# Kernel tuning notes

Hardware: AMD Instinct MI355X
Metric: run time of the kernel (lower is better)

Reference implementation:

```python
import jax, jax.numpy as jnp
import numpy as np

POOL = 7  # RoIPooling output size (7,7)


def roi_pool(x, img, rois):
    """RoIPool matching the torch loop: scale rois to feature coords, truncate to int,
    take inclusive slice [y1:y2+1, x1:x2+1] and AdaptiveMaxPool2d((7,7)).
    x: [1,C,H,W], img: [1,3,h,w], rois: [N,4] (x1,y1,x2,y2 in image coords).
    Returns [N,C,7,7]."""
    _, C, H, W = x.shape
    h_img, w_img = img.shape[2], img.shape[3]
    scale = jnp.array([W / w_img, H / h_img, W / w_img, H / h_img], jnp.float32)
    r = (rois * scale).astype(jnp.int32)  # .long() truncation (coords >= 0)
    x1 = jnp.clip(r[:, 0], 0, W - 1)
    y1 = jnp.clip(r[:, 1], 0, H - 1)
    x2 = jnp.clip(r[:, 2], 0, W - 1)
    y2 = jnp.clip(r[:, 3], 0, H - 1)
    ww = x2 - x1 + 1  # inclusive slice width
    hh = y2 - y1 + 1
    i = jnp.arange(POOL)
    # AdaptiveMaxPool bin boundaries: start=floor(i*L/7), end=ceil((i+1)*L/7)  -> [N,7]
    col_s = x1[:, None] + (i[None, :] * ww[:, None]) // POOL
    col_e = x1[:, None] + ((i[None, :] + 1) * ww[:, None] + POOL - 1) // POOL
    row_s = y1[:, None] + (i[None, :] * hh[:, None]) // POOL
    row_e = y1[:, None] + ((i[None, :] + 1) * hh[:, None] + POOL - 1) // POOL
    wpos = jnp.arange(W)
    hpos = jnp.arange(H)
    colmask = (wpos[None, None, :] >= col_s[:, :, None]) & (wpos[None, None, :] < col_e[:, :, None])  # [N,7,W]
    rowmask = (hpos[None, None, :] >= row_s[:, :, None]) & (hpos[None, None, :] < row_e[:, :, None])  # [N,7,H]
    feat = x[0]  # [C,H,W]
    neg = jnp.asarray(jnp.finfo(feat.dtype).min, feat.dtype)
    def per_roi(masks):
        rm, cm = masks  # [7,H], [7,W]
        # separable max over the rectangular bin: cols first, then rows
        t = jnp.max(jnp.where(cm[None, None, :, :], feat[:, :, None, :], neg), axis=-1)  # [C,H,7]
        return jnp.max(jnp.where(rm[None, :, :, None], t[:, None, :, :], neg), axis=2)  # [C,7,7]
    return jax.lax.map(per_roi, (rowmask, colmask))  # [N,C,7,7]


def setup_inputs() -> dict:
    key = jax.random.key(0)
    ks = jax.random.split(key, 10)
    C, H, W = 512, 50, 50
    h_img, w_img = 800, 800
    N = 512
    num_classes = 20
    x = jax.random.normal(ks[0], (1, C, H, W), jnp.float32)
    img = jnp.zeros((1, 3, h_img, w_img), jnp.float32)
    bx = jax.random.uniform(ks[1], (N,), minval=0.0, maxval=w_img - 320.0)
    by = jax.random.uniform(ks[2], (N,), minval=0.0, maxval=h_img - 320.0)
    bw = jax.random.uniform(ks[3], (N,), minval=32.0, maxval=320.0)
    bh = jax.random.uniform(ks[4], (N,), minval=32.0, maxval=320.0)
    rois = jnp.stack([bx, by, bx + bw, by + bh], axis=1).astype(jnp.float32)
    D = C * POOL * POOL  # 25088
    W1 = jax.random.normal(ks[5], (D, 4096), jnp.float32) / np.sqrt(D)
    b1 = jnp.zeros((4096,), jnp.float32)
    W2 = jax.random.normal(ks[6], (4096, 4096), jnp.float32) / np.sqrt(4096)
    b2 = jnp.zeros((4096,), jnp.float32)
    Wcls = jax.random.normal(ks[7], (4096, num_classes + 1), jnp.float32) / np.sqrt(4096)
    bcls = jnp.zeros((num_classes + 1,), jnp.float32)
    Wreg = jax.random.normal(ks[8], (4096, 4 * (num_classes + 1)), jnp.float32) / np.sqrt(4096)
    breg = jnp.zeros((4 * (num_classes + 1),), jnp.float32)
    return {"x": x, "img": img, "rois": rois, "W1": W1, "b1": b1, "W2": W2,
            "b2": b2, "Wcls": Wcls, "bcls": bcls, "Wreg": Wreg, "breg": breg}


def reference(x, img, rois, W1, b1, W2, b2, Wcls, bcls, Wreg, breg):
    pooled = roi_pool(x, img, rois)                 # [N,C,7,7]
    f = pooled.reshape(pooled.shape[0], -1)          # flatten -> [N,25088]
    f = jax.nn.relu(f @ W1 + b1)                     # fc_head layer 1
    f = jax.nn.relu(f @ W2 + b2)                     # fc_head layer 2
    y_cls = f @ Wcls + bcls                          # [N, num_classes+1]
    y_reg = f @ Wreg + breg                          # [N, 4*(num_classes+1)]
    return (y_cls, y_reg)
```

## Files before the change

kernel.cpp:

```cpp
#include <hip/hip_runtime.h>


typedef __attribute__((ext_vector_type(8))) __bf16 bf16x8;
typedef __attribute__((ext_vector_type(4))) float f32x4;
typedef __attribute__((ext_vector_type(4))) unsigned int u32x4;

#define N_ROIS 512
#define FH 50
#define FW 50
#define KK1 25088
#define D1 4096
#define BK 32

__device__ __forceinline__ void gll16(const void* g, void* l) {
  __builtin_amdgcn_global_load_lds(
      (const __attribute__((address_space(1))) void*)g,
      (__attribute__((address_space(3))) void*)l, 16, 0, 0);
}

__global__ __launch_bounds__(256) void roipool_kernel(
    const float* __restrict__ x, const float* __restrict__ rois,
    __bf16* __restrict__ pooled) {
  const int bid = blockIdx.x;
  const int roi = bid >> 3;
  const int cg = bid & 7;
  const float s = 0.0625f;
  const float r0 = rois[roi * 4 + 0], r1 = rois[roi * 4 + 1];
  const float r2 = rois[roi * 4 + 2], r3 = rois[roi * 4 + 3];
  int x1 = (int)(r0 * s); x1 = min(max(x1, 0), FW - 1);
  int y1 = (int)(r1 * s); y1 = min(max(y1, 0), FH - 1);
  int x2 = (int)(r2 * s); x2 = min(max(x2, 0), FW - 1);
  int y2 = (int)(r3 * s); y2 = min(max(y2, 0), FH - 1);
  const int ww = x2 - x1 + 1, hh = y2 - y1 + 1;
  __shared__ int cs[7], ce[7], rs[7], re[7];
  if (threadIdx.x < 7) {
    int i = threadIdx.x;
    cs[i] = x1 + (i * ww) / 7;
    ce[i] = x1 + ((i + 1) * ww + 6) / 7;
    rs[i] = y1 + (i * hh) / 7;
    re[i] = y1 + ((i + 1) * hh + 6) / 7;
  }
  __syncthreads();
  for (int idx = threadIdx.x; idx < 64 * 49; idx += 256) {
    int cl = idx / 49;
    int p = idx - cl * 49;
    int py = p / 7, px = p - py * 7;
    const int c = cg * 64 + cl;
    const float* base = x + (size_t)c * (FH * FW);
    float m = -3.402823466e38f;
    for (int y = rs[py]; y < re[py]; ++y) {
      const float* rowp = base + y * FW;
      for (int xx = cs[px]; xx < ce[px]; ++xx) m = fmaxf(m, rowp[xx]);
    }
    pooled[(size_t)roi * KK1 + c * 49 + p] = (__bf16)m;
  }
}

template <typename OutT>
__global__ __launch_bounds__(256, 3) void gemm_pipe(
    const __bf16* __restrict__ A, const float* __restrict__ B,
    OutT* __restrict__ part, int N, int K, int kslice, int npad, int zshift) {
  __shared__ unsigned int Bu[2][2048];
  __shared__ __bf16 A_lds[2][128 * 32];
  const int tid = threadIdx.x;
  const int lane = tid & 63;
  const int w = tid >> 6;
  const int wm = w >> 1, wn = w & 1;
  const int bid = blockIdx.x;
  const int z = bid & ((1 << zshift) - 1);
  const int rest = bid >> zshift;
  const int mt = rest & 3;
  const int nt = rest >> 2;
  const int n0 = nt * 128;
  const int m0 = mt * 128;
  const int kbeg = z * kslice;
  const int niters = kslice / BK;
  const int fr = lane & 15;
  const int ks = lane >> 4;

  f32x4 acc[4][4];
#pragma unroll
  for (int i = 0; i < 4; ++i)
#pragma unroll
    for (int j = 0; j < 4; ++j) acc[i][j] = (f32x4){0.f, 0.f, 0.f, 0.f};

  const int aswz = (lane & 3) ^ ((lane >> 2) & 3) ^ ((lane >> 4) & 3);
  const __bf16* Asrc =
      A + (size_t)(m0 + w * 32 + (lane >> 2)) * K + kbeg + aswz * 8;
  const int aslot = ks ^ ((fr & 3) ^ ((fr >> 2) & 3));

  const int bc = tid & 127;
  const int bh = tid >> 7;
  const float* Bgsrc = B + n0 + bc;
  const int bswz = (bc >> 2) & 3;
  const int widx0 = bc * 16 + (((2 * bh) ^ bswz) << 2);
  const int widx1 = bc * 16 + (((2 * bh + 1) ^ bswz) << 2);

  float g0, g1, g2, g3, g4, g5, g6, g7, g8, g9, ga, gb, gc, gd, ge, gf;

#define LOAD_BG(t)                                                        \
  {                                                                       \
    int off = (t) * BK;                                                   \
    if (off >= kslice) off = 0;             \
    const float* p = Bgsrc + (size_t)(kbeg + off + 16 * bh) * N;          \
    g0 = p[0];            g1 = p[(size_t)N];                              \
    g2 = p[(size_t)2*N];  g3 = p[(size_t)3*N];                            \
    g4 = p[(size_t)4*N];  g5 = p[(size_t)5*N];                            \
    g6 = p[(size_t)6*N];  g7 = p[(size_t)7*N];                            \
    g8 = p[(size_t)8*N];  g9 = p[(size_t)9*N];                            \
    ga = p[(size_t)10*N]; gb = p[(size_t)11*N];                           \
    gc = p[(size_t)12*N]; gd = p[(size_t)13*N];                           \
    ge = p[(size_t)14*N]; gf = p[(size_t)15*N];                           \
  }

#define WRITE_BU(buf)                                                     \
  {                                                                       \
    union { __bf16 h[2]; unsigned int u; } q;                             \
    unsigned int u0, u1, u2, u3, u4, u5, u6, u7;                          \
    q.h[0] = (__bf16)g0; q.h[1] = (__bf16)g1; u0 = q.u;                   \
    q.h[0] = (__bf16)g2; q.h[1] = (__bf16)g3; u1 = q.u;                   \
    q.h[0] = (__bf16)g4; q.h[1] = (__bf16)g5; u2 = q.u;                   \
    q.h[0] = (__bf16)g6; q.h[1] = (__bf16)g7; u3 = q.u;                   \
    q.h[0] = (__bf16)g8; q.h[1] = (__bf16)g9; u4 = q.u;                   \
    q.h[0] = (__bf16)ga; q.h[1] = (__bf16)gb; u5 = q.u;                   \
    q.h[0] = (__bf16)gc; q.h[1] = (__bf16)gd; u6 = q.u;                   \
    q.h[0] = (__bf16)ge; q.h[1] = (__bf16)gf; u7 = q.u;                   \
    *(u32x4*)&Bu[buf][widx0] = (u32x4){u0, u1, u2, u3};                   \
    *(u32x4*)&Bu[buf][widx1] = (u32x4){u4, u5, u6, u7};                   \
  }

#define STAGE_A(t)                                                        \
  {                                                                       \
    int off = (t) * BK;                                                   \
    if (off >= kslice) off = 0;    \
    _Pragma("unroll") for (int i = 0; i < 2; ++i) {                       \
      gll16((const void*)(Asrc + (size_t)(i * 16) * K + off),             \
            (void*)&A_lds[(t) & 1][(w * 32 + i * 16) * 32]);              \
    }                                                                     \
  }

  LOAD_BG(0);
  STAGE_A(0);
  WRITE_BU(0);
  __syncthreads();

  for (int it = 0; it < niters; ++it) {
    const int cur = it & 1;
    const bool more = (it + 1) < niters;
    if (more) {
      LOAD_BG(it + 1);
      STAGE_A(it + 1);
    }
    bf16x8 af[4];
    {
      const __bf16* al = &A_lds[cur][0];
#pragma unroll
      for (int mf = 0; mf < 4; ++mf)
        af[mf] = *(const bf16x8*)(al + (wm * 64 + mf * 16 + fr) * 32 +
                                  aslot * 8);
    }
    const unsigned int* bl = &Bu[cur][0];
#pragma unroll
    for (int nf = 0; nf < 4; ++nf) {
      const int c = wn * 64 + nf * 16 + fr;
      bf16x8 bfr = *(const bf16x8*)((const char*)bl + c * 64 +
                                    (ks ^ ((c >> 2) & 3)) * 16);
#pragma unroll
      for (int mf = 0; mf < 4; ++mf)
        acc[mf][nf] = __builtin_amdgcn_mfma_f32_16x16x32_bf16(
            af[mf], bfr, acc[mf][nf], 0, 0, 0);
    }
    if (more) WRITE_BU(cur ^ 1);
    __syncthreads();
  }
#undef STAGE_A
#undef WRITE_BU
#undef LOAD_BG

  const int r0 = ks * 4;
  OutT* pbase = part + (size_t)z * 512 * npad;
#pragma unroll
  for (int mf = 0; mf < 4; ++mf)
#pragma unroll
    for (int nf = 0; nf < 4; ++nf) {
      const int col = n0 + wn * 64 + nf * 16 + fr;
#pragma unroll
      for (int r = 0; r < 4; ++r) {
        const int row = m0 + wm * 64 + mf * 16 + r0 + r;
        pbase[(size_t)row * npad + col] = (OutT)acc[mf][nf][r];
      }
    }
}

template <typename OutT>
__global__ __launch_bounds__(256, 1) void gemm_small(
    const __bf16* __restrict__ A, const float* __restrict__ B,
    OutT* __restrict__ part, int N, int K, int kslice, int npad, int zshift) {
  const int tid = threadIdx.x;
  const int lane = tid & 63;
  const int w = tid >> 6;
  const int bid = blockIdx.x;
  const int z = bid & ((1 << zshift) - 1);
  const int n0 = (bid >> zshift) * 64;
  const int kbeg = z * kslice;
  const int niters = kslice / BK;
  const int kmax = kbeg + kslice;
  const int fr = lane & 15;
  const int ks = lane >> 4;
  const int m0 = w * 128;
  const bool fullN = (n0 + 64) <= N;

  f32x4 acc[8][4];
#pragma unroll
  for (int i = 0; i < 8; ++i)
#pragma unroll
    for (int j = 0; j < 4; ++j) acc[i][j] = (f32x4){0.f, 0.f, 0.f, 0.f};

  const __bf16* Abase = A + (size_t)(m0 + fr) * K + ks * 8;
  const size_t Astride = (size_t)16 * K;
  const float* Bbase = B + n0 + fr;

  bf16x8 afA[8], afB[8];
  float bA[32], bB[32];

#define LOAD_A(D, t)                                                     \
  {                                                                      \
    int kk = kbeg + (t) * BK;                                            \
    if (kk >= kmax) kk = kbeg;                                           \
    const __bf16* ap = Abase + kk;                                       \
    _Pragma("unroll") for (int i = 0; i < 8; ++i)                        \
        D[i] = *(const bf16x8*)(ap + (size_t)i * Astride);               \
  }

#define LOAD_B(S, t)                                                     \
  {                                                                      \
    int kg = kbeg + (t) * BK;                                            \
    if (kg >= kmax) kg = kbeg;                                           \
    const float* p = Bbase + (size_t)(kg + ks * 8) * N;                  \
    if (fullN) {                                                         \
      _Pragma("unroll") for (int e = 0; e < 8; ++e) {                    \
        _Pragma("unroll") for (int nf = 0; nf < 4; ++nf)                 \
            S[e * 4 + nf] = p[nf * 16];                                  \
        p += N;                                                          \
      }                                                                  \
    } else {                                                             \
      _Pragma("unroll") for (int e = 0; e < 8; ++e) {                    \
        _Pragma("unroll") for (int nf = 0; nf < 4; ++nf)                 \
            S[e * 4 + nf] =                                              \
                (n0 + nf * 16 + fr < N) ? p[nf * 16] : 0.f;              \
        p += N;                                                          \
      }                                                                  \
    }                                                                    \
  }

#define BODY(it, CA, NA, CB)                                             \
  {                                                                      \
    bf16x8 bfr[4];                                                       \
    _Pragma("unroll") for (int e = 0; e < 8; ++e)                        \
        _Pragma("unroll") for (int nf = 0; nf < 4; ++nf)                 \
            bfr[nf][e] = (__bf16)CB[e * 4 + nf];                         \
    LOAD_B(CB, (it) + 2);                                                \
    LOAD_A(NA, (it) + 1);                                                \
    _Pragma("unroll") for (int nf = 0; nf < 4; ++nf)                     \
        _Pragma("unroll") for (int mf = 0; mf < 8; ++mf)                 \
            acc[mf][nf] = __builtin_amdgcn_mfma_f32_16x16x32_bf16(       \
                CA[mf], bfr[nf], acc[mf][nf], 0, 0, 0);                  \
  }

  LOAD_A(afA, 0);
  LOAD_B(bA, 0);
  LOAD_B(bB, 1);
  for (int it = 0; it < niters; it += 2) {
    BODY(it, afA, afB, bA);
    BODY(it + 1, afB, afA, bB);
  }
#undef BODY
#undef LOAD_B
#undef LOAD_A

  const int r0 = ks * 4;
  OutT* pbase = part + (size_t)z * 512 * npad;
#pragma unroll
  for (int mf = 0; mf < 8; ++mf)
#pragma unroll
    for (int nf = 0; nf < 4; ++nf) {
      const int col = n0 + nf * 16 + fr;
#pragma unroll
      for (int r = 0; r < 4; ++r) {
        const int row = m0 + mf * 16 + r0 + r;
        pbase[(size_t)row * npad + col] = (OutT)acc[mf][nf][r];
      }
    }
}

__global__ __launch_bounds__(256) void reduce_relu_kernel(
    const __bf16* __restrict__ part, const float* __restrict__ bias,
    __bf16* __restrict__ out, int nsplit) {
  const int idx = blockIdx.x * 256 + threadIdx.x;
  const int flat = idx * 8;
  if (flat >= 512 * 4096) return;
  float s[8];
#pragma unroll
  for (int j = 0; j < 8; ++j) s[j] = 0.f;
  for (int sp = 0; sp < nsplit; ++sp) {
    bf16x8 v = *(const bf16x8*)(part + (size_t)sp * (512 * 4096) + flat);
#pragma unroll
    for (int j = 0; j < 8; ++j) s[j] += (float)v[j];
  }
  const int nb = flat & 4095;
  bf16x8 o;
#pragma unroll
  for (int j = 0; j < 8; ++j) {
    float v = s[j] + bias[nb + j];
    o[j] = (__bf16)(v > 0.f ? v : 0.f);
  }
  *(bf16x8*)(out + flat) = o;
}

__global__ __launch_bounds__(256) void reduce_out_kernel(
    const float* __restrict__ pc, const float* __restrict__ pr,
    const float* __restrict__ bcls, const float* __restrict__ breg,
    float* __restrict__ out, int nsplit) {
  const int gid = blockIdx.x * 256 + threadIdx.x;
  if (gid >= 512 * 105) return;
  if (gid < 512 * 21) {
    const int m = gid / 21, j = gid - m * 21;
    float s = bcls[j];
    for (int sp = 0; sp < nsplit; ++sp)
      s += pc[(size_t)sp * 512 * 128 + m * 128 + j];
    out[gid] = s;
  } else {
    const int g = gid - 512 * 21;
    const int m = g / 84, j = g - m * 84;
    float s = breg[j];
    for (int sp = 0; sp < nsplit; ++sp)
      s += pr[(size_t)sp * 512 * 128 + m * 128 + j];
    out[gid] = s;
  }
}

extern "C" void kernel_launch(void* const* d_in, const int* in_sizes, int n_in,
                              void* d_out, int out_size, void* d_ws, size_t ws_size,
                              hipStream_t stream) {
  (void)in_sizes; (void)n_in; (void)out_size;
  const float* x    = (const float*)d_in[0];
  const float* rois = (const float*)d_in[2];
  const float* W1   = (const float*)d_in[3];
  const float* b1   = (const float*)d_in[4];
  const float* W2   = (const float*)d_in[5];
  const float* b2   = (const float*)d_in[6];
  const float* Wcls = (const float*)d_in[7];
  const float* bcls = (const float*)d_in[8];
  const float* Wreg = (const float*)d_in[9];
  const float* breg = (const float*)d_in[10];
  float* out = (float*)d_out;

  const size_t pooled_b = (size_t)512 * KK1 * 2;
  const size_t act_b = (size_t)512 * D1 * 2;
  const size_t need8 = pooled_b + (size_t)8 * act_b + 2 * act_b;
  const int ns = (ws_size >= need8) ? 8 : 2;
  const int zshift = (ns == 8) ? 3 : 1;

  char* ws = (char*)d_ws;
  __bf16* pooled = (__bf16*)ws;
  __bf16* part1 = (__bf16*)(ws + pooled_b);
  __bf16* f1 = (__bf16*)(ws + pooled_b + (size_t)ns * act_b);
  __bf16* f2 = (__bf16*)(ws + pooled_b + (size_t)ns * act_b + act_b);
  __bf16* part2 = (__bf16*)ws;
  float* pcls = (float*)ws;
  float* preg = (float*)(ws + (size_t)64 * 512 * 128 * 4);

  roipool_kernel<<<N_ROIS * 8, 256, 0, stream>>>(x, rois, pooled);

  gemm_pipe<__bf16><<<32 * 4 * ns, 256, 0, stream>>>(
      pooled, W1, part1, 4096, KK1, KK1 / ns, 4096, zshift);
  reduce_relu_kernel<<<1024, 256, 0, stream>>>(part1, b1, f1, ns);

  gemm_pipe<__bf16><<<32 * 4 * ns, 256, 0, stream>>>(
      f1, W2, part2, 4096, 4096, 4096 / ns, 4096, zshift);
  reduce_relu_kernel<<<1024, 256, 0, stream>>>(part2, b2, f2, ns);

  gemm_small<float><<<64, 256, 0, stream>>>(
      f2, Wcls, pcls, 21, 4096, 64, 128, 6);
  gemm_small<float><<<128, 256, 0, stream>>>(
      f2, Wreg, preg, 84, 4096, 64, 128, 6);
  reduce_out_kernel<<<(512 * 105 + 255) / 256, 256, 0, stream>>>(
      pcls, preg, bcls, breg, out, 64);
}
```

Baseline: 371.3 us.

## Retile FC GEMMs to full-M 512x64 blocks so each weight column is read once

The big FC GEMM kernel now uses 512-thread blocks that each cover all 512 rows (ROIs) and a 64-wide column strip, instead of 128x128 tiles across four M-tiles. The point is that each fp32 weight element is loaded from global memory and converted to bf16 only once, not four times, which cuts the dominant weight traffic. The cost is a larger A tile in LDS, fewer blocks per CU (launch bounds 512,1), and a grid of 64*ns blocks, which may lower occupancy and latency hiding.

```diff
diff --git a/kernel.cpp b/kernel.cpp
--- a/kernel.cpp
+++ b/kernel.cpp
@@ -3,7 +3,6 @@
 
 typedef __attribute__((ext_vector_type(8))) __bf16 bf16x8;
 typedef __attribute__((ext_vector_type(4))) float f32x4;
-typedef __attribute__((ext_vector_type(4))) unsigned int u32x4;
 
 #define N_ROIS 512
 #define FH 50
@@ -57,22 +56,17 @@
 }
 
 template <typename OutT>
-__global__ __launch_bounds__(256, 3) void gemm_pipe(
+__global__ __launch_bounds__(512, 1) void gemm_pipe(
     const __bf16* __restrict__ A, const float* __restrict__ B,
     OutT* __restrict__ part, int N, int K, int kslice, int npad, int zshift) {
-  __shared__ unsigned int Bu[2][2048];
-  __shared__ __bf16 A_lds[2][128 * 32];
+  __shared__ __bf16 A_lds[2][512 * 32];
+  __shared__ unsigned int Bu[2][1024];
   const int tid = threadIdx.x;
   const int lane = tid & 63;
   const int w = tid >> 6;
-  const int wm = w >> 1, wn = w & 1;
   const int bid = blockIdx.x;
   const int z = bid & ((1 << zshift) - 1);
-  const int rest = bid >> zshift;
-  const int mt = rest & 3;
-  const int nt = rest >> 2;
-  const int n0 = nt * 128;
-  const int m0 = mt * 128;
+  const int n0 = (bid >> zshift) * 64;
   const int kbeg = z * kslice;
   const int niters = kslice / BK;
   const int fr = lane & 15;
@@ -86,56 +80,44 @@
 
   const int aswz = (lane & 3) ^ ((lane >> 2) & 3) ^ ((lane >> 4) & 3);
   const __bf16* Asrc =
-      A + (size_t)(m0 + w * 32 + (lane >> 2)) * K + kbeg + aswz * 8;
+      A + (size_t)(w * 64 + (lane >> 2)) * K + kbeg + aswz * 8;
   const int aslot = ks ^ ((fr & 3) ^ ((fr >> 2) & 3));
 
-  const int bc = tid & 127;
-  const int bh = tid >> 7;
+  const int bc = tid & 63;
+  const int bh = tid >> 6;
   const float* Bgsrc = B + n0 + bc;
-  const int bswz = (bc >> 2) & 3;
-  const int widx0 = bc * 16 + (((2 * bh) ^ bswz) << 2);
-  const int widx1 = bc * 16 + (((2 * bh + 1) ^ bswz) << 2);
-
-  float g0, g1, g2, g3, g4, g5, g6, g7, g8, g9, ga, gb, gc, gd, ge, gf;
+  const int kp0 = 2 * bh;
+  const int widx = bc * 16 + (((kp0 >> 2) ^ ((bc >> 2) & 3)) << 2) + (kp0 & 3);
+
+  float g0, g1, g2, g3;
 
 #define LOAD_BG(t)                                                        \
   {                                                                       \
     int off = (t) * BK;                                                   \
     if (off >= kslice) off = 0;             \
-    const float* p = Bgsrc + (size_t)(kbeg + off + 16 * bh) * N;          \
-    g0 = p[0];            g1 = p[(size_t)N];                              \
-    g2 = p[(size_t)2*N];  g3 = p[(size_t)3*N];                            \
-    g4 = p[(size_t)4*N];  g5 = p[(size_t)5*N];                            \
-    g6 = p[(size_t)6*N];  g7 = p[(size_t)7*N];                            \
-    g8 = p[(size_t)8*N];  g9 = p[(size_t)9*N];                            \
-    ga = p[(size_t)10*N]; gb = p[(size_t)11*N];                           \
-    gc = p[(size_t)12*N]; gd = p[(size_t)13*N];                           \
-    ge = p[(size_t)14*N]; gf = p[(size_t)15*N];                           \
+    const float* p = Bgsrc + (size_t)(kbeg + off + 4 * bh) * N;           \
+    g0 = p[0];                                                            \
+    g1 = p[(size_t)N];                                                    \
+    g2 = p[(size_t)2 * N];                                                \
+    g3 = p[(size_t)3 * N];                                                \
   }
 
 #define WRITE_BU(buf)                                                     \
   {                                                                       \
-    union { __bf16 h[2]; unsigned int u; } q;                             \
-    unsigned int u0, u1, u2, u3, u4, u5, u6, u7;                          \
-    q.h[0] = (__bf16)g0; q.h[1] = (__bf16)g1; u0 = q.u;                   \
-    q.h[0] = (__bf16)g2; q.h[1] = (__bf16)g3; u1 = q.u;                   \
-    q.h[0] = (__bf16)g4; q.h[1] = (__bf16)g5; u2 = q.u;                   \
-    q.h[0] = (__bf16)g6; q.h[1] = (__bf16)g7; u3 = q.u;                   \
-    q.h[0] = (__bf16)g8; q.h[1] = (__bf16)g9; u4 = q.u;                   \
-    q.h[0] = (__bf16)ga; q.h[1] = (__bf16)gb; u5 = q.u;                   \
-    q.h[0] = (__bf16)gc; q.h[1] = (__bf16)gd; u6 = q.u;                   \
-    q.h[0] = (__bf16)ge; q.h[1] = (__bf16)gf; u7 = q.u;                   \
-    *(u32x4*)&Bu[buf][widx0] = (u32x4){u0, u1, u2, u3};                   \
-    *(u32x4*)&Bu[buf][widx1] = (u32x4){u4, u5, u6, u7};                   \
+    union { __bf16 h[2]; unsigned int u; } q0, q1;                        \
+    q0.h[0] = (__bf16)g0; q0.h[1] = (__bf16)g1;                           \
+    q1.h[0] = (__bf16)g2; q1.h[1] = (__bf16)g3;                           \
+    *(unsigned long long*)&Bu[buf][widx] =                                \
+        ((unsigned long long)q1.u << 32) | q0.u;                          \
   }
 
 #define STAGE_A(t)                                                        \
   {                                                                       \
     int off = (t) * BK;                                                   \
     if (off >= kslice) off = 0;    \
-    _Pragma("unroll") for (int i = 0; i < 2; ++i) {                       \
+    _Pragma("unroll") for (int i = 0; i < 4; ++i) {                       \
       gll16((const void*)(Asrc + (size_t)(i * 16) * K + off),             \
-            (void*)&A_lds[(t) & 1][(w * 32 + i * 16) * 32]);              \
+            (void*)&A_lds[(t) & 1][(w * 64 + i * 16) * 32]);              \
     }                                                                     \
   }
 
@@ -156,13 +138,13 @@
       const __bf16* al = &A_lds[cur][0];
 #pragma unroll
       for (int mf = 0; mf < 4; ++mf)
-        af[mf] = *(const bf16x8*)(al + (wm * 64 + mf * 16 + fr) * 32 +
+        af[mf] = *(const bf16x8*)(al + (w * 64 + mf * 16 + fr) * 32 +
                                   aslot * 8);
     }
     const unsigned int* bl = &Bu[cur][0];
 #pragma unroll
     for (int nf = 0; nf < 4; ++nf) {
-      const int c = wn * 64 + nf * 16 + fr;
+      const int c = nf * 16 + fr;
       bf16x8 bfr = *(const bf16x8*)((const char*)bl + c * 64 +
                                     (ks ^ ((c >> 2) & 3)) * 16);
 #pragma unroll
@@ -183,10 +165,10 @@
   for (int mf = 0; mf < 4; ++mf)
 #pragma unroll
     for (int nf = 0; nf < 4; ++nf) {
-      const int col = n0 + wn * 64 + nf * 16 + fr;
+      const int col = n0 + nf * 16 + fr;
 #pragma unroll
       for (int r = 0; r < 4; ++r) {
-        const int row = m0 + wm * 64 + mf * 16 + r0 + r;
+        const int row = w * 64 + mf * 16 + r0 + r;
         pbase[(size_t)row * npad + col] = (OutT)acc[mf][nf][r];
       }
     }
@@ -372,11 +354,11 @@
 
   roipool_kernel<<<N_ROIS * 8, 256, 0, stream>>>(x, rois, pooled);
 
-  gemm_pipe<__bf16><<<32 * 4 * ns, 256, 0, stream>>>(
+  gemm_pipe<__bf16><<<64 * ns, 512, 0, stream>>>(
       pooled, W1, part1, 4096, KK1, KK1 / ns, 4096, zshift);
   reduce_relu_kernel<<<1024, 256, 0, stream>>>(part1, b1, f1, ns);
 
-  gemm_pipe<__bf16><<<32 * 4 * ns, 256, 0, stream>>>(
+  gemm_pipe<__bf16><<<64 * ns, 512, 0, stream>>>(
       f1, W2, part2, 4096, 4096, 4096 / ns, 4096, zshift);
   reduce_relu_kernel<<<1024, 256, 0, stream>>>(part2, b2, f2, ns);
 
```

Result: slower. 395.1 us (+6.4%).
